# Kernel tuning notes

Measured on AMD Instinct MI355X. Metric: run time of the kernel, lower is better.

Reference implementation:

```python
import jax, jax.numpy as jnp
import numpy as np

WINDOW_SIZES = [4, 8, 12]
BN_EPS = 1e-5


def conv1x1(x, w, b):
    # x: [B,C,H,W], w: [O,C], b: [O]
    return jnp.einsum('bchw,oc->bohw', x, w) + b[None, :, None, None]


def bnorm(x, gamma, beta, mean, var):
    inv = gamma * jax.lax.rsqrt(var + BN_EPS)
    return (x - mean[None, :, None, None]) * inv[None, :, None, None] + beta[None, :, None, None]


def shift5(x):
    # ShiftConv2d1 depthwise fixed-weight conv == 4-direction zero-padded shift + identity
    b, c, H, W = x.shape
    g = c // 5
    p = jnp.pad(x, ((0, 0), (0, 0), (1, 1), (1, 1)))
    return jnp.concatenate([
        p[:, 0 * g:1 * g, 1:-1, 2:],    # kernel[1,2]: x[i, j+1]
        p[:, 1 * g:2 * g, 1:-1, :-2],   # kernel[1,0]: x[i, j-1]
        p[:, 2 * g:3 * g, 2:, 1:-1],    # kernel[2,1]: x[i+1, j]
        p[:, 3 * g:4 * g, :-2, 1:-1],   # kernel[0,1]: x[i-1, j]
        p[:, 4 * g:, 1:-1, 1:-1],       # kernel[1,1]: identity
    ], axis=1)


def lfe(x, w0, b0, w1, b1):
    y = jax.nn.relu(conv1x1(shift5(x), w0, b0))
    return conv1x1(shift5(y), w1, b1)


def win_part(x, ws):
    # [B,C,H,W] -> [B*nh*nw, ws*ws, C]
    b, c, H, W = x.shape
    x = x.reshape(b, c, H // ws, ws, W // ws, ws)
    return x.transpose(0, 2, 4, 3, 5, 1).reshape(b * (H // ws) * (W // ws), ws * ws, c)


def win_merge(y, ws, b, H, W):
    # [B*nh*nw, ws*ws, C] -> [B,C,H,W]
    c = y.shape[-1]
    y = y.reshape(b, H // ws, W // ws, ws, ws, c)
    return y.transpose(0, 5, 1, 3, 2, 4).reshape(b, c, H, W)


def gmsa_first(x, pi_w, pi_b, bn_g, bn_b, bn_m, bn_v, po_w, po_b):
    b, c, H, W = x.shape
    xp = bnorm(conv1x1(x, pi_w, pi_b), bn_g, bn_b, bn_m, bn_v)
    ch = 2 * c // 3
    ys, atns = [], []
    for i, ws in enumerate(WINDOW_SIZES):
        x_ = xp[:, i * ch:(i + 1) * ch]
        x_ = jnp.roll(x_, (-(ws // 2), -(ws // 2)), axis=(2, 3))
        qv = win_part(x_, ws)                      # [nw, ws*ws, 2*cc]
        cc = ch // 2
        q, v = qv[..., :cc], qv[..., cc:]
        atn = jax.nn.softmax(q @ q.transpose(0, 2, 1), axis=-1)
        y_ = win_merge(atn @ v, ws, b, H, W)
        y_ = jnp.roll(y_, (ws // 2, ws // 2), axis=(2, 3))
        ys.append(y_)
        atns.append(atn)
    return conv1x1(jnp.concatenate(ys, axis=1), po_w, po_b), atns


def gmsa_shared(x, atns, pi_w, pi_b, bn_g, bn_b, bn_m, bn_v, po_w, po_b):
    b, c, H, W = x.shape
    xp = bnorm(conv1x1(x, pi_w, pi_b), bn_g, bn_b, bn_m, bn_v)
    ch = c // 3
    ys = []
    for i, ws in enumerate(WINDOW_SIZES):
        x_ = jnp.roll(xp[:, i * ch:(i + 1) * ch], (-(ws // 2), -(ws // 2)), axis=(2, 3))
        v = win_part(x_, ws)
        y_ = win_merge(atns[i] @ v, ws, b, H, W)
        ys.append(jnp.roll(y_, (ws // 2, ws // 2), axis=(2, 3)))
    return conv1x1(jnp.concatenate(ys, axis=1), po_w, po_b)


def setup_inputs() -> dict:
    key = jax.random.key(0)
    ks = jax.random.split(key, 20)
    B, C, H, W = 4, 60, 384, 384
    E = 2 * C  # exp_ratio=2 hidden width
    s = 0.05

    def rn(k, shape):
        return jax.random.normal(k, shape, dtype=jnp.float32) * s

    return {
        'x': jax.random.normal(ks[0], (B, C, H, W), dtype=jnp.float32),
        # LFE 0
        'lfe0_w0': rn(ks[1], (E, C)), 'lfe0_b0': jnp.zeros((E,), jnp.float32),
        'lfe0_w1': rn(ks[2], (C, E)), 'lfe0_b1': jnp.zeros((C,), jnp.float32),
        # GMSA 0 (calc_attn=True): project_inp C->2C, BN(2C), project_out C->C
        'g0_pi_w': rn(ks[3], (2 * C, C)), 'g0_pi_b': jnp.zeros((2 * C,), jnp.float32),
        'g0_bn_g': jnp.ones((2 * C,), jnp.float32), 'g0_bn_b': jnp.zeros((2 * C,), jnp.float32),
        'g0_bn_m': jnp.zeros((2 * C,), jnp.float32), 'g0_bn_v': jnp.ones((2 * C,), jnp.float32),
        'g0_po_w': rn(ks[4], (C, C)), 'g0_po_b': jnp.zeros((C,), jnp.float32),
        # LFE 1
        'lfe1_w0': rn(ks[5], (E, C)), 'lfe1_b0': jnp.zeros((E,), jnp.float32),
        'lfe1_w1': rn(ks[6], (C, E)), 'lfe1_b1': jnp.zeros((C,), jnp.float32),
        # GMSA 1 (calc_attn=False): project_inp C->C, BN(C), project_out C->C
        'g1_pi_w': rn(ks[7], (C, C)), 'g1_pi_b': jnp.zeros((C,), jnp.float32),
        'g1_bn_g': jnp.ones((C,), jnp.float32), 'g1_bn_b': jnp.zeros((C,), jnp.float32),
        'g1_bn_m': jnp.zeros((C,), jnp.float32), 'g1_bn_v': jnp.ones((C,), jnp.float32),
        'g1_po_w': rn(ks[8], (C, C)), 'g1_po_b': jnp.zeros((C,), jnp.float32),
    }


def reference(x, lfe0_w0, lfe0_b0, lfe0_w1, lfe0_b1,
              g0_pi_w, g0_pi_b, g0_bn_g, g0_bn_b, g0_bn_m, g0_bn_v, g0_po_w, g0_po_b,
              lfe1_w0, lfe1_b0, lfe1_w1, lfe1_b1,
              g1_pi_w, g1_pi_b, g1_bn_g, g1_bn_b, g1_bn_m, g1_bn_v, g1_po_w, g1_po_b):
    # depth 0
    x = lfe(x, lfe0_w0, lfe0_b0, lfe0_w1, lfe0_b1) + x
    y, atns = gmsa_first(x, g0_pi_w, g0_pi_b, g0_bn_g, g0_bn_b, g0_bn_m, g0_bn_v, g0_po_w, g0_po_b)
    x = y + x
    # shared depth 1 (reuses attention maps)
    x = lfe(x, lfe1_w0, lfe1_b0, lfe1_w1, lfe1_b1) + x
    y = gmsa_shared(x, atns, g1_pi_w, g1_pi_b, g1_bn_g, g1_bn_b, g1_bn_m, g1_bn_v, g1_po_w, g1_po_b)
    return y + x
```

## Files before the change

### kernel.cpp

```cpp
#include <hip/hip_runtime.h>
#include <math.h>

constexpr int B_ = 4, C_ = 60, H_ = 384, W_ = 384;
constexpr int HW_ = H_ * W_;
constexpr int NC_ = B_ * C_ * HW_;
constexpr int NE_ = B_ * 120 * HW_;

typedef __attribute__((ext_vector_type(8))) short short8;
typedef __attribute__((ext_vector_type(4))) float f32x4;
typedef __attribute__((ext_vector_type(4))) unsigned short u16x4;

__device__ __forceinline__ unsigned short f2b(float f) {
    unsigned u = __builtin_bit_cast(unsigned, f);
    unsigned r = (u + 0x7fff + ((u >> 16) & 1)) >> 16;
    return (unsigned short)r;
}
__device__ __forceinline__ float b2f(unsigned short s) {
    return __builtin_bit_cast(float, (unsigned)s << 16);
}

struct PrepJobs {
    const float* src[8];
    unsigned short* dst[8];
    int cin[8];
    int cout[8];
};

__global__ __launch_bounds__(256) void prep_all(PrepJobs J)
{
    int bid = blockIdx.x;
    #pragma unroll 1
    for (int j = 0; j < 8; ++j) {
        const int KP = J.cin[j]  > 64 ? 128 : 64;
        const int MP = J.cout[j] > 64 ? 128 : 64;
        const int nb = MP * KP / 256;
        if (bid < nb) {
            const int i = bid * 256 + threadIdx.x;
            const int o = i / KP, c = i - o * KP;
            const float v = (o < J.cout[j] && c < J.cin[j]) ? J.src[j][o * J.cin[j] + c] : 0.f;
            J.dst[j][o * KP + (c ^ ((o & 7) << 3))] = f2b(v);
            return;
        }
        bid -= nb;
    }
}

struct ABJobs {
    const float* bias[8];
    const float* g[8];
    const float* bb[8];
    const float* m[8];
    const float* v[8];
    float* dst[8];
    int cout[8];
};

__global__ __launch_bounds__(256) void prep_ab(ABJobs J)
{
    const int j = blockIdx.x;
    const int n = J.cout[j];
    for (int o = threadIdx.x; o < n; o += 256) {
        float A = 1.f, Bv = J.bias[j][o];
        if (J.g[j]) {
            const float s = J.g[j][o] * rsqrtf(J.v[j][o] + 1e-5f);
            A  = s;
            Bv = (Bv - J.m[j][o]) * s + J.bb[j][o];
        }
        J.dst[j][o]     = A;
        J.dst[j][n + o] = Bv;
    }
}

template<int KP>
__device__ __forceinline__ int lds_off(int px, int cb) {
    return px * (KP * 2) + (cb ^ ((px & 7) << 4) ^ (((px >> 3) & 1) << 6));
}

template<int CIN, int COUT, int GSH, bool SRCB, bool RELU, bool RESID,
         bool RESIDB, bool OUTB, bool EXTRACT>
__global__ __launch_bounds__(256, 4)
void conv_g(const void* __restrict__ in_, const unsigned short* __restrict__ wp,
            const float* __restrict__ AB,
            const void* __restrict__ resid_, void* __restrict__ out_,
            unsigned short* __restrict__ q0)
{
    constexpr int KP  = CIN  > 64 ? 128 : 64;
    constexpr int MP  = COUT > 64 ? 128 : 64;
    constexpr int NNT = MP / 16;
    constexpr int KBL = KP / 32;
    __shared__ __align__(16) char xlds[128 * KP * 2];

    const int tid = threadIdx.x;
    const int n0  = blockIdx.x * 128;
    const int b   = n0 / HW_;
    const int p0  = n0 - b * HW_;
    const int hh  = p0 / W_;
    const int ww0 = p0 - hh * W_;

    for (int task = tid; task < (KP / 2) * 16; task += 256) {
        const int oct = (task >> 4) & 15;
        const int pr  = (task & 15) | ((task >> 8) << 4);
        const int c0  = pr * 2;
        const int s0  = oct * 8;

        if (c0 >= CIN) {
            #pragma unroll
            for (int i = 0; i < 8; ++i)
                *(unsigned*)(xlds + lds_off<KP>(s0 + i, c0 * 2)) = 0u;
            continue;
        }

        int dh = 0, dw = 0;
        if (GSH > 0) {
            const int grp = c0 / GSH;
            dh = (grp == 2) ? 1 : ((grp == 3) ? -1 : 0);
            dw = (grp == 0) ? 1 : ((grp == 1) ? -1 : 0);
        }
        const int h2 = hh + dh;
        const bool vh = (unsigned)h2 < (unsigned)H_;
        const long eoff = (long)(b * CIN + c0) * HW_ + h2 * W_ + ww0 + s0;

        unsigned short va[8], vb[8];
        if (vh) {
            if constexpr (SRCB) {
                const unsigned short* p = (const unsigned short*)in_;
                short8 A = *(const short8*)(p + eoff);
                short8 Bv = *(const short8*)(p + eoff + HW_);
                #pragma unroll
                for (int i = 0; i < 8; ++i) { va[i] = (unsigned short)A[i]; vb[i] = (unsigned short)Bv[i]; }
            } else {
                const float* p = (const float*)in_;
                f32x4 A0 = *(const f32x4*)(p + eoff);
                f32x4 A1 = *(const f32x4*)(p + eoff + 4);
                f32x4 B0 = *(const f32x4*)(p + eoff + HW_);
                f32x4 B1 = *(const f32x4*)(p + eoff + HW_ + 4);
                #pragma unroll
                for (int i = 0; i < 4; ++i) {
                    va[i] = f2b(A0[i]); va[i + 4] = f2b(A1[i]);
                    vb[i] = f2b(B0[i]); vb[i + 4] = f2b(B1[i]);
                }
            }
        } else {
            #pragma unroll
            for (int i = 0; i < 8; ++i) { va[i] = 0; vb[i] = 0; }
        }
        #pragma unroll
        for (int i = 0; i < 8; ++i) {
            const int px = s0 + i - dw;
            if ((unsigned)px < 128u) {
                const unsigned v = (unsigned)va[i] | ((unsigned)vb[i] << 16);
                *(unsigned*)(xlds + lds_off<KP>(px, c0 * 2)) = v;
            }
        }
        if (GSH > 0 && dw != 0) {
            const bool hndl = (dw == 1) ? (oct == 15) : (oct == 0);
            if (hndl) {
                const int px_e = (dw == 1) ? 127 : 0;
                const int w_abs = ww0 + px_e + dw;
                unsigned short ua = 0, ub = 0;
                if (vh && (unsigned)w_abs < (unsigned)W_) {
                    const long e2 = (long)(b * CIN + c0) * HW_ + h2 * W_ + w_abs;
                    if constexpr (SRCB) {
                        ua = ((const unsigned short*)in_)[e2];
                        ub = ((const unsigned short*)in_)[e2 + HW_];
                    } else {
                        ua = f2b(((const float*)in_)[e2]);
                        ub = f2b(((const float*)in_)[e2 + HW_]);
                    }
                }
                *(unsigned*)(xlds + lds_off<KP>(px_e, c0 * 2)) =
                    (unsigned)ua | ((unsigned)ub << 16);
            }
        }
    }
    __syncthreads();

    const int wv = tid >> 6, lo = tid & 15, hi = (tid & 63) >> 4;
    f32x4 acc[2][NNT];
    #pragma unroll
    for (int mt = 0; mt < 2; ++mt)
        #pragma unroll
        for (int nt = 0; nt < NNT; ++nt) acc[mt][nt] = f32x4{0.f, 0.f, 0.f, 0.f};

    #pragma unroll
    for (int kb = 0; kb < KBL; ++kb) {
        short8 a[2], bb[NNT];
        #pragma unroll
        for (int mt = 0; mt < 2; ++mt) {
            const int row = wv * 32 + mt * 16 + lo;
            a[mt] = *(const short8*)(xlds + lds_off<KP>(row, kb * 64 + hi * 16));
        }
        #pragma unroll
        for (int nt = 0; nt < NNT; ++nt) {
            const int row = nt * 16 + lo;
            bb[nt] = *(const short8*)((const char*)wp +
                      row * (KP * 2) + ((kb * 64 + hi * 16) ^ ((row & 7) << 4)));
        }
        #pragma unroll
        for (int mt = 0; mt < 2; ++mt)
            #pragma unroll
            for (int nt = 0; nt < NNT; ++nt)
                acc[mt][nt] = __builtin_amdgcn_mfma_f32_16x16x32_bf16(
                    a[mt], bb[nt], acc[mt][nt], 0, 0, 0);
    }

    #pragma unroll
    for (int mt = 0; mt < 2; ++mt) {
        const int px0 = p0 + wv * 32 + mt * 16 + hi * 4;
        #pragma unroll
        for (int nt = 0; nt < NNT; ++nt) {
            const int ch = nt * 16 + lo;
            if (ch < COUT) {
                const long oi = (long)(b * COUT + ch) * HW_ + px0;
                float v[4];
                f32x4 rf;
                u16x4 rb;
                if (RESID) {
                    if (RESIDB) rb = *(const u16x4*)((const unsigned short*)resid_ + oi);
                    else        rf = *(const f32x4*)((const float*)resid_ + oi);
                }
                #pragma unroll
                for (int r = 0; r < 4; ++r) {
                    float t = fmaf(acc[mt][nt][r], AB[ch], AB[COUT + ch]);
                    if (RELU) t = fmaxf(t, 0.f);
                    if (RESID) t += RESIDB ? b2f(rb[r]) : rf[r];
                    v[r] = t;
                }
                if (OUTB) {
                    u16x4 o4;
                    #pragma unroll
                    for (int r = 0; r < 4; ++r) o4[r] = f2b(v[r]);
                    *(u16x4*)((unsigned short*)out_ + oi) = o4;
                } else {
                    *(f32x4*)((float*)out_ + oi) = f32x4{v[0], v[1], v[2], v[3]};
                }
                if (EXTRACT) {
                    const int wi = ch / 40, rr = ch - wi * 40;
                    if (rr < 20) {
                        u16x4 o4;
                        #pragma unroll
                        for (int r = 0; r < 4; ++r) o4[r] = f2b(v[r]);
                        *(u16x4*)(q0 + (long)(b * 60 + wi * 20 + rr) * HW_ + px0) = o4;
                    }
                }
            }
        }
    }
}

template<int WS, int WPB>
__global__ __launch_bounds__(256)
void attn_m(const unsigned short* __restrict__ qsrc, int qC, int qbase,
            const unsigned short* __restrict__ vsrc, int vC, int vbase,
            unsigned short* __restrict__ out, int obase)
{
    constexpr int P     = WS * WS;
    constexpr int NMT   = P / 16;
    constexpr int S     = WS / 2;
    constexpr int WGX   = W_ / WS;
    constexpr int WGY   = H_ / WS;
    constexpr int QP    = 40;
    constexpr int KP2   = ((P + 31) / 32) * 32;
    constexpr int VP    = KP2 + 8;
    constexpr int KB2   = KP2 / 32;
    constexpr int TILES = WPB * NMT;

    __shared__ __align__(16) unsigned short Qs[WPB * P * QP];
    __shared__ __align__(16) unsigned short VTs[WPB * 32 * VP];
    __shared__ __align__(16) unsigned short Ps[WPB * P * VP];
    __shared__ float rs[WPB * P];

    const int tid = threadIdx.x;

    for (int i = tid; i < WPB * P * 6; i += 256) {
        const int row = i / 6, j = i - (i / 6) * 6;
        *(unsigned*)&Qs[row * QP + 20 + 2 * j] = 0u;
    }
    for (int i = tid; i < WPB * 12 * (KP2 / 2); i += 256) {
        const int rr = i / (KP2 / 2), j = i - rr * (KP2 / 2);
        const int win = rr / 12, ch = 20 + (rr - (rr / 12) * 12);
        *(unsigned*)&VTs[(win * 32 + ch) * VP + 2 * j] = 0u;
    }
    if constexpr (KP2 > P) {
        for (int i = tid; i < WPB * 20 * ((KP2 - P) / 2); i += 256) {
            const int rr = i / ((KP2 - P) / 2), j = i - rr * ((KP2 - P) / 2);
            const int win = rr / 20, ch = rr - (rr / 20) * 20;
            *(unsigned*)&VTs[(win * 32 + ch) * VP + P + 2 * j] = 0u;
        }
        for (int i = tid; i < WPB * P * ((KP2 - P) / 2); i += 256) {
            const int row = i / ((KP2 - P) / 2), j = i - row * ((KP2 - P) / 2);
            *(unsigned*)&Ps[row * VP + P + 2 * j] = 0u;
        }
    }
    for (int e = tid; e < WPB * P * 20; e += 256) {
        const int win = e / (P * 20);
        const int rem = e - win * (P * 20);
        const int ch  = rem / P;
        const int pos = rem - ch * P;
        const int gw  = blockIdx.x * WPB + win;
        const int b   = gw / (WGY * WGX);
        const int rwin = gw - b * (WGY * WGX);
        const int wh = rwin / WGX, ww = rwin - (rwin / WGX) * WGX;
        const int pr = pos / WS,  pc = pos - (pos / WS) * WS;
        int hs = wh * WS + pr + S; if (hs >= H_) hs -= H_;
        int wd = ww * WS + pc + S; if (wd >= W_) wd -= W_;
        const long off = (long)hs * W_ + wd;
        Qs [(win * P  + pos) * QP + ch ] = qsrc[(long)(b * qC + qbase + ch) * HW_ + off];
        VTs[(win * 32 + ch ) * VP + pos] = vsrc[(long)(b * vC + vbase + ch) * HW_ + off];
    }
    __syncthreads();

    const int wv = tid >> 6, lo = tid & 15, hi = (tid & 63) >> 4;

    for (int t = wv; t < TILES; t += 4) {
        const int win = t / NMT, mt = t - (t / NMT) * NMT;
        const unsigned short* Qw = Qs + win * P * QP;
        unsigned short* Pw = Ps + win * P * VP;

        const short8 af = *(const short8*)(Qw + (mt * 16 + lo) * QP + hi * 8);
        f32x4 a1[NMT];
        #pragma unroll
        for (int nt = 0; nt < NMT; ++nt) a1[nt] = f32x4{0.f, 0.f, 0.f, 0.f};
        #pragma unroll
        for (int nt = 0; nt < NMT; ++nt) {
            const short8 bf = *(const short8*)(Qw + (nt * 16 + lo) * QP + hi * 8);
            a1[nt] = __builtin_amdgcn_mfma_f32_16x16x32_bf16(af, bf, a1[nt], 0, 0, 0);
        }
        float psum[4] = {0.f, 0.f, 0.f, 0.f};
        #pragma unroll
        for (int nt = 0; nt < NMT; ++nt) {
            #pragma unroll
            for (int r = 0; r < 4; ++r) {
                const float p = __expf(a1[nt][r]);
                psum[r] += p;
                Pw[(mt * 16 + hi * 4 + r) * VP + nt * 16 + lo] = f2b(p);
            }
        }
        #pragma unroll
        for (int r = 0; r < 4; ++r) {
            psum[r] += __shfl_xor(psum[r], 1);
            psum[r] += __shfl_xor(psum[r], 2);
            psum[r] += __shfl_xor(psum[r], 4);
            psum[r] += __shfl_xor(psum[r], 8);
        }
        if (lo == 0) {
            #pragma unroll
            for (int r = 0; r < 4; ++r)
                rs[win * P + mt * 16 + hi * 4 + r] = psum[r];
        }
    }
    __syncthreads();

    for (int t = wv; t < TILES; t += 4) {
        const int win = t / NMT, qt = t - (t / NMT) * NMT;
        const unsigned short* Vw = VTs + win * 32 * VP;
        const unsigned short* Pw = Ps + win * P * VP;

        f32x4 a2[2];
        a2[0] = f32x4{0.f, 0.f, 0.f, 0.f};
        a2[1] = f32x4{0.f, 0.f, 0.f, 0.f};
        #pragma unroll
        for (int kb = 0; kb < KB2; ++kb) {
            const short8 bf = *(const short8*)(Pw + (qt * 16 + lo) * VP + kb * 32 + hi * 8);
            #pragma unroll
            for (int m2 = 0; m2 < 2; ++m2) {
                const short8 af = *(const short8*)(Vw + (m2 * 16 + lo) * VP + kb * 32 + hi * 8);
                a2[m2] = __builtin_amdgcn_mfma_f32_16x16x32_bf16(af, bf, a2[m2], 0, 0, 0);
            }
        }
        const int gw = blockIdx.x * WPB + win;
        const int b  = gw / (WGY * WGX);
        const int rwin = gw - b * (WGY * WGX);
        const int wh = rwin / WGX, ww = rwin - (rwin / WGX) * WGX;

        const int row = qt * 16 + lo;
        const float inv = 1.f / rs[win * P + row];
        const int pr = row / WS, pc = row - (row / WS) * WS;
        int hs = wh * WS + pr + S; if (hs >= H_) hs -= H_;
        int wd = ww * WS + pc + S; if (wd >= W_) wd -= W_;
        const long pbase = (long)(b * 60 + obase) * HW_ + (long)hs * W_ + wd;
        #pragma unroll
        for (int m2 = 0; m2 < 2; ++m2) {
            #pragma unroll
            for (int r = 0; r < 4; ++r) {
                const int ch = m2 * 16 + hi * 4 + r;
                if (ch < 20)
                    out[pbase + (long)ch * HW_] = f2b(a2[m2][r] * inv);
            }
        }
    }
}

extern "C" void kernel_launch(void* const* d_in, const int* in_sizes, int n_in,
                              void* d_out, int out_size, void* d_ws, size_t ws_size,
                              hipStream_t stream)
{
    const float* x     = (const float*)d_in[0];
    const float* l0w0  = (const float*)d_in[1];
    const float* l0b0  = (const float*)d_in[2];
    const float* l0w1  = (const float*)d_in[3];
    const float* l0b1  = (const float*)d_in[4];
    const float* g0piw = (const float*)d_in[5];
    const float* g0pib = (const float*)d_in[6];
    const float* g0bng = (const float*)d_in[7];
    const float* g0bnb = (const float*)d_in[8];
    const float* g0bnm = (const float*)d_in[9];
    const float* g0bnv = (const float*)d_in[10];
    const float* g0pow = (const float*)d_in[11];
    const float* g0pob = (const float*)d_in[12];
    const float* l1w0  = (const float*)d_in[13];
    const float* l1b0  = (const float*)d_in[14];
    const float* l1w1  = (const float*)d_in[15];
    const float* l1b1  = (const float*)d_in[16];
    const float* g1piw = (const float*)d_in[17];
    const float* g1pib = (const float*)d_in[18];
    const float* g1bng = (const float*)d_in[19];
    const float* g1bnb = (const float*)d_in[20];
    const float* g1bnm = (const float*)d_in[21];
    const float* g1bnv = (const float*)d_in[22];
    const float* g1pow = (const float*)d_in[23];
    const float* g1pob = (const float*)d_in[24];

    unsigned short* HID = (unsigned short*)d_ws;
    unsigned short* XPB = HID + NE_;
    unsigned short* Q0  = XPB + NE_;
    unsigned short* CCB = Q0 + NC_;
    unsigned short* WP  = CCB + NC_;
    float*          ABF = (float*)(WP + 53248);
    unsigned short* YS1 = XPB + NC_;
    float* OUTF  = (float*)d_out;
    unsigned short* YS0 = (unsigned short*)d_out;

    unsigned short* W1  = WP;
    unsigned short* W2  = WP + 8192;
    unsigned short* W3  = WP + 16384;
    unsigned short* W5  = WP + 24576;
    unsigned short* W6  = WP + 28672;
    unsigned short* W7  = WP + 36864;
    unsigned short* W8  = WP + 45056;
    unsigned short* W10 = WP + 49152;

    float* AB1  = ABF;
    float* AB2  = ABF + 240;
    float* AB3  = ABF + 360;
    float* AB5  = ABF + 600;
    float* AB6  = ABF + 720;
    float* AB7  = ABF + 960;
    float* AB8  = ABF + 1080;
    float* AB10 = ABF + 1200;

    PrepJobs J;
    J.src[0]=l0w0;  J.dst[0]=W1;  J.cin[0]=60;  J.cout[0]=120;
    J.src[1]=l0w1;  J.dst[1]=W2;  J.cin[1]=120; J.cout[1]=60;
    J.src[2]=g0piw; J.dst[2]=W3;  J.cin[2]=60;  J.cout[2]=120;
    J.src[3]=g0pow; J.dst[3]=W5;  J.cin[3]=60;  J.cout[3]=60;
    J.src[4]=l1w0;  J.dst[4]=W6;  J.cin[4]=60;  J.cout[4]=120;
    J.src[5]=l1w1;  J.dst[5]=W7;  J.cin[5]=120; J.cout[5]=60;
    J.src[6]=g1piw; J.dst[6]=W8;  J.cin[6]=60;  J.cout[6]=60;
    J.src[7]=g1pow; J.dst[7]=W10; J.cin[7]=60;  J.cout[7]=60;
    prep_all<<<208, 256, 0, stream>>>(J);

    ABJobs A;
    for (int j = 0; j < 8; ++j) { A.g[j]=nullptr; A.bb[j]=nullptr; A.m[j]=nullptr; A.v[j]=nullptr; }
    A.bias[0]=l0b0;  A.dst[0]=AB1;  A.cout[0]=120;
    A.bias[1]=l0b1;  A.dst[1]=AB2;  A.cout[1]=60;
    A.bias[2]=g0pib; A.dst[2]=AB3;  A.cout[2]=120; A.g[2]=g0bng; A.bb[2]=g0bnb; A.m[2]=g0bnm; A.v[2]=g0bnv;
    A.bias[3]=g0pob; A.dst[3]=AB5;  A.cout[3]=60;
    A.bias[4]=l1b0;  A.dst[4]=AB6;  A.cout[4]=120;
    A.bias[5]=l1b1;  A.dst[5]=AB7;  A.cout[5]=60;
    A.bias[6]=g1pib; A.dst[6]=AB8;  A.cout[6]=60;  A.g[6]=g1bng; A.bb[6]=g1bnb; A.m[6]=g1bnm; A.v[6]=g1bnv;
    A.bias[7]=g1pob; A.dst[7]=AB10; A.cout[7]=60;
    prep_ab<<<8, 256, 0, stream>>>(A);

    dim3 blk(256);
    dim3 gconv(B_ * HW_ / 128);

    conv_g<60,120,12,false,true,false,false,true,false><<<gconv,blk,0,stream>>>(
        x, W1, AB1, nullptr, HID, nullptr);
    conv_g<120,60,24,true,false,true,false,true,false><<<gconv,blk,0,stream>>>(
        HID, W2, AB2, x, CCB, nullptr);
    conv_g<60,120,0,true,false,false,false,true,true><<<gconv,blk,0,stream>>>(
        CCB, W3, AB3, nullptr, XPB, Q0);
    attn_m<4,4><<<dim3(9216),blk,0,stream>>>(XPB,120,0,   XPB,120,20,  YS0, 0);
    attn_m<8,1><<<dim3(9216),blk,0,stream>>>(XPB,120,40,  XPB,120,60,  YS0,20);
    attn_m<12,1><<<dim3(4096),blk,0,stream>>>(XPB,120,80, XPB,120,100, YS0,40);
    conv_g<60,60,0,true,false,true,true,true,false><<<gconv,blk,0,stream>>>(
        YS0, W5, AB5, CCB, CCB, nullptr);
    conv_g<60,120,12,true,true,false,false,true,false><<<gconv,blk,0,stream>>>(
        CCB, W6, AB6, nullptr, HID, nullptr);
    conv_g<120,60,24,true,false,true,true,true,false><<<gconv,blk,0,stream>>>(
        HID, W7, AB7, CCB, CCB, nullptr);
    conv_g<60,60,0,true,false,false,false,true,false><<<gconv,blk,0,stream>>>(
        CCB, W8, AB8, nullptr, XPB, nullptr);
    attn_m<4,4><<<dim3(9216),blk,0,stream>>>(Q0,60,0,  XPB,60,0,  YS1, 0);
    attn_m<8,1><<<dim3(9216),blk,0,stream>>>(Q0,60,20, XPB,60,20, YS1,20);
    attn_m<12,1><<<dim3(4096),blk,0,stream>>>(Q0,60,40, XPB,60,40, YS1,40);
    conv_g<60,60,0,true,false,true,true,false,false><<<gconv,blk,0,stream>>>(
        YS1, W10, AB10, CCB, OUTF, nullptr);
}
```

Before: 1.199 ms.

## Vectorize attention window gather and drop separate Q0 extraction buffer

The attention kernel's window load now has each thread read four contiguous bf16 values from a window row with one 64-bit load, instead of one scalar element per thread. Windows that wrap around the image edge fall back to a scalar loop. The EXTRACT epilogue that copied the first-stage Q channels into a separate Q0 buffer is removed. The shared-attention stage now reads Q directly from the retained XPB projection, and the second projection goes to a new XP1 buffer. This removes extra global writes and uncoalesced scalar gathers, at the cost of keeping a larger buffer alive and some index arithmetic and divergence in the load loop.

```diff
diff --git a/kernel.cpp b/kernel.cpp
--- a/kernel.cpp
+++ b/kernel.cpp
@@ -77,12 +77,11 @@
 }
 
 template<int CIN, int COUT, int GSH, bool SRCB, bool RELU, bool RESID,
-         bool RESIDB, bool OUTB, bool EXTRACT>
+         bool RESIDB, bool OUTB>
 __global__ __launch_bounds__(256, 4)
 void conv_g(const void* __restrict__ in_, const unsigned short* __restrict__ wp,
             const float* __restrict__ AB,
-            const void* __restrict__ resid_, void* __restrict__ out_,
-            unsigned short* __restrict__ q0)
+            const void* __restrict__ resid_, void* __restrict__ out_)
 {
     constexpr int KP  = CIN  > 64 ? 128 : 64;
     constexpr int MP  = COUT > 64 ? 128 : 64;
@@ -234,15 +233,6 @@
                 } else {
                     *(f32x4*)((float*)out_ + oi) = f32x4{v[0], v[1], v[2], v[3]};
                 }
-                if (EXTRACT) {
-                    const int wi = ch / 40, rr = ch - wi * 40;
-                    if (rr < 20) {
-                        u16x4 o4;
-                        #pragma unroll
-                        for (int r = 0; r < 4; ++r) o4[r] = f2b(v[r]);
-                        *(u16x4*)(q0 + (long)(b * 60 + wi * 20 + rr) * HW_ + px0) = o4;
-                    }
-                }
             }
         }
     }
@@ -259,11 +249,13 @@
     constexpr int S     = WS / 2;
     constexpr int WGX   = W_ / WS;
     constexpr int WGY   = H_ / WS;
+    constexpr int NWIN  = WGY * WGX;
     constexpr int QP    = 40;
     constexpr int KP2   = ((P + 31) / 32) * 32;
     constexpr int VP    = KP2 + 8;
     constexpr int KB2   = KP2 / 32;
     constexpr int TILES = WPB * NMT;
+    constexpr int NG    = (WS + 6) / 4;
 
     __shared__ __align__(16) unsigned short Qs[WPB * P * QP];
     __shared__ __align__(16) unsigned short VTs[WPB * 32 * VP];
@@ -292,21 +284,46 @@
             *(unsigned*)&Ps[row * VP + P + 2 * j] = 0u;
         }
     }
-    for (int e = tid; e < WPB * P * 20; e += 256) {
-        const int win = e / (P * 20);
-        const int rem = e - win * (P * 20);
-        const int ch  = rem / P;
-        const int pos = rem - ch * P;
-        const int gw  = blockIdx.x * WPB + win;
-        const int b   = gw / (WGY * WGX);
-        const int rwin = gw - b * (WGY * WGX);
-        const int wh = rwin / WGX, ww = rwin - (rwin / WGX) * WGX;
-        const int pr = pos / WS,  pc = pos - (pos / WS) * WS;
-        int hs = wh * WS + pr + S; if (hs >= H_) hs -= H_;
-        int wd = ww * WS + pc + S; if (wd >= W_) wd -= W_;
-        const long off = (long)hs * W_ + wd;
-        Qs [(win * P  + pos) * QP + ch ] = qsrc[(long)(b * qC + qbase + ch) * HW_ + off];
-        VTs[(win * 32 + ch ) * VP + pos] = vsrc[(long)(b * vC + vbase + ch) * HW_ + off];
+
+    for (int t = tid; t < WPB * 2 * 20 * WS * NG; t += 256) {
+        int r = t;
+        const int g    = r % NG; r /= NG;
+        const int wrow = r % WS; r /= WS;
+        const int ch   = r % 20; r /= 20;
+        const int tens = r & 1;  r >>= 1;
+        const int win  = r;
+
+        const int gw   = blockIdx.x * WPB + win;
+        const int b    = gw / NWIN;
+        const int rwin = gw - b * NWIN;
+        const int wh   = rwin / WGX, ww = rwin - (rwin / WGX) * WGX;
+        int hs = wh * WS + wrow + S; if (hs >= H_) hs -= H_;
+        const int c0 = ww * WS + S;
+        const unsigned short* src = tens ? vsrc : qsrc;
+        const int cc = tens ? (vC * b + vbase) : (qC * b + qbase);
+        const long rowbase = (long)(cc + ch) * HW_ + (long)hs * W_;
+
+        if (c0 + WS <= W_) {
+            const int col0 = (c0 & ~3) + 4 * g;
+            const u16x4 v4 = *(const u16x4*)(src + rowbase + col0);
+            #pragma unroll
+            for (int e = 0; e < 4; ++e) {
+                const int pc = col0 + e - c0;
+                if ((unsigned)pc < (unsigned)WS) {
+                    const int pos = wrow * WS + pc;
+                    if (tens) VTs[(win * 32 + ch) * VP + pos] = v4[e];
+                    else      Qs [(win * P + pos) * QP + ch]  = v4[e];
+                }
+            }
+        } else if (g == 0) {
+            for (int pc = 0; pc < WS; ++pc) {
+                int wd = c0 + pc; if (wd >= W_) wd -= W_;
+                const unsigned short u = src[rowbase + wd];
+                const int pos = wrow * WS + pc;
+                if (tens) VTs[(win * 32 + ch) * VP + pos] = u;
+                else      Qs [(win * P + pos) * QP + ch]  = u;
+            }
+        }
     }
     __syncthreads();
 
@@ -369,8 +386,8 @@
             }
         }
         const int gw = blockIdx.x * WPB + win;
-        const int b  = gw / (WGY * WGX);
-        const int rwin = gw - b * (WGY * WGX);
+        const int b  = gw / NWIN;
+        const int rwin = gw - b * NWIN;
         const int wh = rwin / WGX, ww = rwin - (rwin / WGX) * WGX;
 
         const int row = qt * 16 + lo;
@@ -423,11 +440,11 @@
 
     unsigned short* HID = (unsigned short*)d_ws;
     unsigned short* XPB = HID + NE_;
-    unsigned short* Q0  = XPB + NE_;
-    unsigned short* CCB = Q0 + NC_;
+    unsigned short* XP1 = XPB + NE_;
+    unsigned short* YS1 = XP1 + NC_;
+    unsigned short* CCB = YS1 + NC_;
     unsigned short* WP  = CCB + NC_;
     float*          ABF = (float*)(WP + 53248);
-    unsigned short* YS1 = XPB + NC_;
     float* OUTF  = (float*)d_out;
     unsigned short* YS0 = (unsigned short*)d_out;
 
@@ -475,26 +492,26 @@
     dim3 blk(256);
     dim3 gconv(B_ * HW_ / 128);
 
-    conv_g<60,120,12,false,true,false,false,true,false><<<gconv,blk,0,stream>>>(
-        x, W1, AB1, nullptr, HID, nullptr);
-    conv_g<120,60,24,true,false,true,false,true,false><<<gconv,blk,0,stream>>>(
-        HID, W2, AB2, x, CCB, nullptr);
-    conv_g<60,120,0,true,false,false,false,true,true><<<gconv,blk,0,stream>>>(
-        CCB, W3, AB3, nullptr, XPB, Q0);
+    conv_g<60,120,12,false,true,false,false,true><<<gconv,blk,0,stream>>>(
+        x, W1, AB1, nullptr, HID);
+    conv_g<120,60,24,true,false,true,false,true><<<gconv,blk,0,stream>>>(
+        HID, W2, AB2, x, CCB);
+    conv_g<60,120,0,true,false,false,false,true><<<gconv,blk,0,stream>>>(
+        CCB, W3, AB3, nullptr, XPB);
     attn_m<4,4><<<dim3(9216),blk,0,stream>>>(XPB,120,0,   XPB,120,20,  YS0, 0);
     attn_m<8,1><<<dim3(9216),blk,0,stream>>>(XPB,120,40,  XPB,120,60,  YS0,20);
     attn_m<12,1><<<dim3(4096),blk,0,stream>>>(XPB,120,80, XPB,120,100, YS0,40);
-    conv_g<60,60,0,true,false,true,true,true,false><<<gconv,blk,0,stream>>>(
-        YS0, W5, AB5, CCB, CCB, nullptr);
-    conv_g<60,120,12,true,true,false,false,true,false><<<gconv,blk,0,stream>>>(
-        CCB, W6, AB6, nullptr, HID, nullptr);
-    conv_g<120,60,24,true,false,true,true,true,false><<<gconv,blk,0,stream>>>(
-        HID, W7, AB7, CCB, CCB, nullptr);
-    conv_g<60,60,0,true,false,false,false,true,false><<<gconv,blk,0,stream>>>(
-        CCB, W8, AB8, nullptr, XPB, nullptr);
-    attn_m<4,4><<<dim3(9216),blk,0,stream>>>(Q0,60,0,  XPB,60,0,  YS1, 0);
-    attn_m<8,1><<<dim3(9216),blk,0,stream>>>(Q0,60,20, XPB,60,20, YS1,20);
-    attn_m<12,1><<<dim3(4096),blk,0,stream>>>(Q0,60,40, XPB,60,40, YS1,40);
-    conv_g<60,60,0,true,false,true,true,false,false><<<gconv,blk,0,stream>>>(
-        YS1, W10, AB10, CCB, OUTF, nullptr);
-}
+    conv_g<60,60,0,true,false,true,true,true><<<gconv,blk,0,stream>>>(
+        YS0, W5, AB5, CCB, CCB);
+    conv_g<60,120,12,true,true,false,false,true><<<gconv,blk,0,stream>>>(
+        CCB, W6, AB6, nullptr, HID);
+    conv_g<120,60,24,true,false,true,true,true><<<gconv,blk,0,stream>>>(
+        HID, W7, AB7, CCB, CCB);
+    conv_g<60,60,0,true,false,false,false,true><<<gconv,blk,0,stream>>>(
+        CCB, W8, AB8, nullptr, XP1);
+    attn_m<4,4><<<dim3(9216),blk,0,stream>>>(XPB,120,0,  XP1,60,0,  YS1, 0);
+    attn_m<8,1><<<dim3(9216),blk,0,stream>>>(XPB,120,40, XP1,60,20, YS1,20);
+    attn_m<12,1><<<dim3(4096),blk,0,stream>>>(XPB,120,80,XP1,60,40, YS1,40);
+    conv_g<60,60,0,true,false,true,true,false><<<gconv,blk,0,stream>>>(
+        YS1, W10, AB10, CCB, OUTF);
+}
```

Result: slower. 1.301 ms (+8.5%).
